# Kernel optimization log

Hardware: AMD Instinct MI355X
Metric: run time of the kernel (lower is better)

The kernel has to match this reference:

```python
import jax, jax.numpy as jnp
import numpy as np

N_PHM = 4  # hypercomplex division


def _kron_weight(phm_rule, W, in_f, out_f):
    # phm_rule: [n, n, n], W: [n, in_f//n, out_f//n]
    # W_full[p*in_n + q, r*out_n + s] = sum_i phm_rule[i,p,r] * W[i,q,s]
    Wf = jnp.einsum('ipr,iqs->pqrs', phm_rule, W)
    return Wf.reshape(in_f, out_f)


def setup_inputs() -> dict:
    key = jax.random.key(0)
    ks = jax.random.split(key, 5)
    T, D, B = 8192, 2048, 512  # tokens, model dim, bottleneck
    n = N_PHM
    x = jax.random.normal(ks[0], (T, D), dtype=jnp.float32)
    phm_rule = jax.random.normal(ks[1], (n, n, n), dtype=jnp.float32) * 0.5
    # glorot-ish scaling for the per-component weights
    W_down = jax.random.normal(ks[2], (n, D // n, B // n), dtype=jnp.float32) * (1.0 / np.sqrt(D))
    b_down = jnp.zeros((B,), dtype=jnp.float32)
    W_up = jax.random.normal(ks[3], (n, B // n, D // n), dtype=jnp.float32) * (1.0 / np.sqrt(B))
    b_up = jnp.zeros((D,), dtype=jnp.float32)
    return {"x": x, "phm_rule": phm_rule, "W_down": W_down, "b_down": b_down,
            "W_up": W_up, "b_up": b_up}


def reference(x, phm_rule, W_down, b_down, W_up, b_up):
    T, D = x.shape
    B = b_down.shape[0]
    Wd = _kron_weight(phm_rule, W_down, D, B)   # [D, B]
    Wu = _kron_weight(phm_rule, W_up, B, D)     # [B, D]
    z = jax.nn.relu(x @ Wd + b_down)            # down-proj + activation
    return z @ Wu + b_up                         # up-proj
```

## Files before the change

### kernel.cpp

```cpp
#include <hip/hip_runtime.h>
#include <hip/hip_bf16.h>
#include <stdint.h>

using bf16 = __hip_bfloat16;
typedef __attribute__((ext_vector_type(8))) short bf16x8;
typedef __attribute__((ext_vector_type(4))) float f32x4;

static __device__ __forceinline__ float b2f(short u) {
  union { float f; unsigned int i; } c;
  c.i = ((unsigned int)(unsigned short)u) << 16;
  return c.f;
}
static __device__ __forceinline__ short f2b(float f) {
  return (short)__bfloat16_as_ushort(__float2bfloat16(f));
}

static __device__ __forceinline__ void cfence() { asm volatile("" ::: "memory"); }
static __device__ __forceinline__ void bar()    { cfence(); __builtin_amdgcn_s_barrier(); cfence(); }

__device__ __forceinline__ void async16(const void* g, void* lds) {
  __builtin_amdgcn_global_load_lds(
      (const __attribute__((address_space(1))) void*)g,
      (__attribute__((address_space(3))) void*)lds, 16, 0, 0);
}

__global__ void build_w(const float* __restrict__ phm,
                        const float* __restrict__ Wd,
                        const float* __restrict__ Wu,
                        bf16* __restrict__ wdT, bf16* __restrict__ wuT) {
  int idx = blockIdx.x * 256 + threadIdx.x;
  if (idx < 1024 * 1024) {
    int n = idx >> 11, k = idx & 2047;
    int r = n >> 7, s = n & 127;
    int p = k >> 9, q = k & 511;
    float v = 0.f;
#pragma unroll
    for (int i = 0; i < 4; ++i)
      v += phm[i * 16 + p * 4 + r] * Wd[i * 65536 + q * 128 + s];
    wdT[idx] = (bf16)v;
  } else {
    int j = idx - 1024 * 1024;
    int d = j >> 9, b = j & 511;
    int r = d >> 9, s = d & 511;
    int p = b >> 7, q = b & 127;
    float v = 0.f;
#pragma unroll
    for (int i = 0; i < 4; ++i)
      v += phm[i * 16 + p * 4 + r] * Wu[i * 65536 + q * 512 + s];
    wuT[j] = (bf16)v;
  }
}

__global__ void zred(const bf16* __restrict__ P, const float* __restrict__ bias,
                     bf16* __restrict__ z) {
  int i = blockIdx.x * 256 + threadIdx.x;
  const int NV = 8192 * 512 / 8;
  if (i >= NV) return;
  const size_t CS = (size_t)NV;
  bf16x8 v0 = ((const bf16x8*)P)[i];
  bf16x8 v1 = ((const bf16x8*)P)[i + CS];
  bf16x8 v2 = ((const bf16x8*)P)[i + 2 * CS];
  bf16x8 v3 = ((const bf16x8*)P)[i + 3 * CS];
  int c0 = (i * 8) & 511;
  bf16x8 o;
#pragma unroll
  for (int j = 0; j < 8; ++j) {
    float t = b2f(v0[j]) + b2f(v1[j]) + b2f(v2[j]) + b2f(v3[j]) + bias[c0 + j];
    o[j] = f2b(t > 0.f ? t : 0.f);
  }
  ((bf16x8*)z)[i] = o;
}

__global__ __launch_bounds__(512, 2)
void gemm1f(const float* __restrict__ X, const bf16* __restrict__ Wt,
            bf16* __restrict__ P) {
  constexpr int BK = 64, KTOT = 2048, NOUT = 512;
  __shared__ bf16 Ash[128 * 64];
  __shared__ bf16 Bsh[2][2][256 * 64];

  const int xcd = blockIdx.x & 7, w = blockIdx.x >> 3;
  const int bx = xcd * 8 + (w & 7);
  const int ch = w >> 3;
  const int bm = bx * 128;
  const int koff = ch * 512;
  bf16* __restrict__ Pc = P + (size_t)ch * 8192 * NOUT;

  const int tid  = threadIdx.x;
  const int lane = tid & 63;
  const int wave = tid >> 6;
  const int wm   = (wave >> 2) * 64;
  const int wnn  = (wave & 3) * 128;
  const int hB   = wnn >> 8;
  const int bb   = wnn & 255;
  const int rl   = lane & 15;
  const int sw   = lane >> 4;
  const int sx   = rl & 7;

  const int arow = tid >> 2;
  const int ac0  = (tid & 3) * 16;
  const float* __restrict__ Xrow = X + (size_t)(bm + arow) * KTOT + koff + ac0;
  const int as0 = (tid & 3) * 2;

  f32x4 acc[4][8] = {};
  float4 av[4];

#define ISSUE_AV(tt)                                                          \
  { _Pragma("unroll")                                                         \
    for (int j = 0; j < 4; ++j)                                               \
      av[j] = *(const float4*)(Xrow + (size_t)(tt) * BK + j * 4); }

#define WRITE_A()                                                             \
  {                                                                           \
    bf16x8 w0, w1;                                                            \
    _Pragma("unroll")                                                         \
    for (int e = 0; e < 4; ++e) {                                             \
      w0[e]     = f2b(((const float*)&av[0])[e]);                             \
      w0[e + 4] = f2b(((const float*)&av[1])[e]);                             \
      w1[e]     = f2b(((const float*)&av[2])[e]);                             \
      w1[e + 4] = f2b(((const float*)&av[3])[e]);                             \
    }                                                                         \
    *(bf16x8*)(&Ash[arow * 64 + (((as0)     ^ (arow & 7)) * 8)]) = w0;        \
    *(bf16x8*)(&Ash[arow * 64 + (((as0 + 1) ^ (arow & 7)) * 8)]) = w1;        \
  }

#define STAGE_BH(tt, h)                                                       \
  { _Pragma("unroll")                                                         \
    for (int is = 0; is < 4; ++is) {                                          \
      int idx = is * 512 + tid;                                               \
      int r = idx >> 3, sl = idx & 7;                                         \
      async16(Wt + (size_t)((h) * 256 + r) * KTOT + koff + (tt) * BK          \
                  + ((sl ^ (r & 7)) * 8),                                     \
              &Bsh[(tt) & 1][h][idx * 8]);                                    \
    } }

  const int nt = 512 / BK;

  ISSUE_AV(0);
  STAGE_BH(0, 0); STAGE_BH(0, 1);
  asm volatile("s_waitcnt vmcnt(8)" ::: "memory");
  WRITE_A();
  ISSUE_AV(1);
  asm volatile("s_waitcnt vmcnt(4) lgkmcnt(0)" ::: "memory");
  bar();

  bf16x8 af[4][2], bfr[2][2];

  for (int t = 0; t < nt; ++t) {
    const int cur = t & 1;
    const bf16* __restrict__ Bcur = &Bsh[cur][hB][0];

#define LDAF(m, ks) af[m][ks] = *(const bf16x8*)(&Ash[(wm + (m)*16 + rl) * 64 + ((((ks)*4 + sw) ^ sx) * 8)])
#define LDBF(j, n, ks) bfr[j][ks] = *(const bf16x8*)(Bcur + (bb + (n)*16 + rl) * 64 + ((((ks)*4 + sw) ^ sx) * 8))
#define QUAD(N0)                                                              \
  __builtin_amdgcn_s_setprio(1);                                              \
  _Pragma("unroll") for (int m = 0; m < 4; ++m)                               \
  _Pragma("unroll") for (int n = 0; n < 2; ++n)                               \
  _Pragma("unroll") for (int ks = 0; ks < 2; ++ks)                            \
    acc[m][(N0) + n] = __builtin_amdgcn_mfma_f32_16x16x32_bf16(               \
        af[m][ks], bfr[n][ks], acc[m][(N0) + n], 0, 0, 0);                    \
  __builtin_amdgcn_s_setprio(0);

    LDAF(0, 0); LDAF(0, 1); LDAF(1, 0); LDAF(1, 1);
    LDAF(2, 0); LDAF(2, 1); LDAF(3, 0); LDAF(3, 1);
    LDBF(0, 0, 0); LDBF(0, 0, 1); LDBF(1, 1, 0); LDBF(1, 1, 1);
    cfence();
    if (t + 1 < nt) STAGE_BH(t + 1, 0);
    bar(); QUAD(0); bar();
    LDBF(0, 2, 0); LDBF(0, 2, 1); LDBF(1, 3, 0); LDBF(1, 3, 1);
    cfence();
    if (t + 1 < nt) STAGE_BH(t + 1, 1);
    bar(); QUAD(2); bar();
    LDBF(0, 4, 0); LDBF(0, 4, 1); LDBF(1, 5, 0); LDBF(1, 5, 1);
    cfence();
    bar(); QUAD(4); bar();
    LDBF(0, 6, 0); LDBF(0, 6, 1); LDBF(1, 7, 0); LDBF(1, 7, 1);
    cfence();
    if (t + 1 < nt) {
      asm volatile("s_waitcnt vmcnt(8)" ::: "memory");
      WRITE_A();
      if (t + 2 < nt) {
        ISSUE_AV(t + 2);
        asm volatile("s_waitcnt vmcnt(4) lgkmcnt(0)" ::: "memory");
      } else {
        asm volatile("s_waitcnt vmcnt(0) lgkmcnt(0)" ::: "memory");
      }
    }
    __builtin_amdgcn_sched_barrier(0);
    bar(); QUAD(6);
    if (t + 1 < nt) bar();

#undef LDAF
#undef LDBF
#undef QUAD
  }
#undef ISSUE_AV
#undef WRITE_A
#undef STAGE_BH

  float* scr = (float*)(&Bsh[0][0][0]) + wave * (16 * 128);
#pragma unroll
  for (int m = 0; m < 4; ++m) {
    int grow = bm + wm + m * 16;
#pragma unroll
    for (int n = 0; n < 8; ++n)
#pragma unroll
      for (int j = 0; j < 4; ++j)
        scr[(sw * 4 + j) * 128 + n * 16 + rl] = acc[m][n][j];
    asm volatile("s_waitcnt lgkmcnt(0)" ::: "memory");
#pragma unroll
    for (int p = 0; p < 4; ++p) {
      int row = p * 4 + sw;
      f32x4 a = *(const f32x4*)(scr + row * 128 + rl * 8);
      f32x4 b = *(const f32x4*)(scr + row * 128 + rl * 8 + 4);
      bf16x8 o;
#pragma unroll
      for (int e = 0; e < 4; ++e) { o[e] = f2b(a[e]); o[e + 4] = f2b(b[e]); }
      *(bf16x8*)(&Pc[(size_t)(grow + row) * NOUT + wnn + rl * 8]) = o;
    }
    asm volatile("s_waitcnt lgkmcnt(0)" ::: "memory");
  }
}

__global__ __launch_bounds__(512, 2)
void gemm2(const bf16* __restrict__ A, const bf16* __restrict__ Bt,
           const float* __restrict__ bias, float* __restrict__ Cout) {
  constexpr int BK = 64, LDA = 512, LDB = 512, N = 2048;
  __shared__ bf16 Ash[2][2][128 * 64];
  __shared__ bf16 Bsh[2][2][128 * 64];

  const int xcd = blockIdx.x & 7, w = blockIdx.x >> 3;
  const int bx = xcd * 4 + (w & 3);
  const int by = w >> 2;
  const int bm = bx * 256;
  const int bn = by * 256;

  const int tid  = threadIdx.x;
  const int lane = tid & 63;
  const int wave = tid >> 6;
  const int wmh  = wave >> 2;
  const int wn   = wave & 3;
  const int wnh  = wn >> 1;
  const int brow = (wn & 1) * 64;
  const int rl   = lane & 15;
  const int sw   = lane >> 4;
  const int sx   = rl & 7;

  f32x4 acc[8][4] = {};

#define STAGE_A(tt, h)                                                        \
  { _Pragma("unroll")                                                         \
    for (int is = 0; is < 2; ++is) {                                          \
      int idx = is * 512 + tid;                                               \
      int r = idx >> 3, sl = idx & 7;                                         \
      async16(A + (size_t)(bm + (h) * 128 + r) * LDA + (tt) * BK              \
                  + ((sl ^ (r & 7)) * 8),                                     \
              &Ash[(tt) & 1][h][idx * 8]);                                    \
    } }
#define STAGE_B(tt, h)                                                        \
  { _Pragma("unroll")                                                         \
    for (int is = 0; is < 2; ++is) {                                          \
      int idx = is * 512 + tid;                                               \
      int r = idx >> 3, sl = idx & 7;                                         \
      async16(Bt + (size_t)(bn + (h) * 128 + r) * LDB + (tt) * BK             \
                  + ((sl ^ (r & 7)) * 8),                                     \
              &Bsh[(tt) & 1][h][idx * 8]);                                    \
    } }

  const int nt = 512 / BK;

  STAGE_A(0, 0); STAGE_A(0, 1);
  STAGE_B(0, 0); STAGE_B(0, 1);
  STAGE_A(1, 0); STAGE_A(1, 1);
  asm volatile("s_waitcnt vmcnt(4)" ::: "memory");
  bar();

  bf16x8 af[8][2], bf[4][2];

  for (int t = 0; t < nt; ++t) {
    const int cur = t & 1;
    const bf16* __restrict__ Acur = &Ash[cur][wmh][0];
    const bf16* __restrict__ Bcur = &Bsh[cur][wnh][0];

#define LDA_(m, ks) af[m][ks] = *(const bf16x8*)(Acur + ((m)*16 + rl) * 64 + ((((ks)*4 + sw) ^ sx) * 8))
#define LDB_(n, ks) bf[n][ks] = *(const bf16x8*)(Bcur + (brow + (n)*16 + rl) * 64 + ((((ks)*4 + sw) ^ sx) * 8))
#define QUAD(M0, N0)                                                          \
  __builtin_amdgcn_s_setprio(1);                                              \
  _Pragma("unroll") for (int m = 0; m < 4; ++m)                               \
  _Pragma("unroll") for (int n = 0; n < 2; ++n)                               \
  _Pragma("unroll") for (int ks = 0; ks < 2; ++ks)                            \
    acc[(M0) + m][(N0) + n] = __builtin_amdgcn_mfma_f32_16x16x32_bf16(        \
        af[(M0) + m][ks], bf[(N0) + n][ks], acc[(M0) + m][(N0) + n], 0, 0, 0);\
  __builtin_amdgcn_s_setprio(0);

    LDA_(0, 0); LDA_(0, 1); LDA_(1, 0); LDA_(1, 1);
    LDA_(2, 0); LDA_(2, 1); LDA_(3, 0); LDA_(3, 1);
    LDB_(0, 0); LDB_(0, 1); LDB_(1, 0); LDB_(1, 1);
    cfence();
    if (t + 1 < nt) STAGE_B(t + 1, 0);
    bar(); QUAD(0, 0); bar();
    LDB_(2, 0); LDB_(2, 1); LDB_(3, 0); LDB_(3, 1);
    cfence();
    if (t + 1 < nt) STAGE_B(t + 1, 1);
    bar(); QUAD(0, 2); bar();
    LDA_(4, 0); LDA_(4, 1); LDA_(5, 0); LDA_(5, 1);
    LDA_(6, 0); LDA_(6, 1); LDA_(7, 0); LDA_(7, 1);
    cfence();
    bar(); QUAD(4, 0); bar();
    if (t + 2 < nt) {
      STAGE_A(t + 2, 0); STAGE_A(t + 2, 1);
      asm volatile("s_waitcnt vmcnt(4)" ::: "memory");
    } else if (t + 1 < nt) {
      asm volatile("s_waitcnt vmcnt(0)" ::: "memory");
    }
    bar(); QUAD(4, 2);
    if (t + 1 < nt) bar();

#undef LDA_
#undef LDB_
#undef QUAD
  }
#undef STAGE_A
#undef STAGE_B

  float* scr = (float*)(&Ash[0][0][0]) + wave * (16 * 68);
  const int r4 = lane >> 4;
  const int c4 = lane & 15;
#pragma unroll
  for (int m = 0; m < 8; ++m) {
    int grow = bm + wmh * 128 + m * 16;
#pragma unroll
    for (int n = 0; n < 4; ++n)
#pragma unroll
      for (int j = 0; j < 4; ++j)
        scr[(sw * 4 + j) * 68 + n * 16 + rl] = acc[m][n][j] + bias[bn + wn * 64 + n * 16 + rl];
    asm volatile("s_waitcnt lgkmcnt(0)" ::: "memory");
#pragma unroll
    for (int jj = 0; jj < 4; ++jj) {
      int row = jj * 4 + r4;
      f32x4 v = *(const f32x4*)(scr + row * 68 + c4 * 4);
      *(f32x4*)(&Cout[(size_t)(grow + row) * N + bn + wn * 64 + c4 * 4]) = v;
    }
    asm volatile("s_waitcnt lgkmcnt(0)" ::: "memory");
  }
}

extern "C" void kernel_launch(void* const* d_in, const int* in_sizes, int n_in,
                              void* d_out, int out_size, void* d_ws, size_t ws_size,
                              hipStream_t stream) {
  const float* x      = (const float*)d_in[0];
  const float* phm    = (const float*)d_in[1];
  const float* W_down = (const float*)d_in[2];
  const float* b_down = (const float*)d_in[3];
  const float* W_up   = (const float*)d_in[4];
  const float* b_up   = (const float*)d_in[5];
  float* out = (float*)d_out;

  const int T = 8192, B = 512;
  const size_t MB = 1024 * 1024;

  char* ws = (char*)d_ws;
  bf16* wdT = (bf16*)(ws);
  bf16* wuT = (bf16*)(ws + 2 * MB);
  bf16* z   = (bf16*)(ws + 4 * MB);
  bf16* P   = (bf16*)(ws + 12 * MB);

  build_w<<<dim3((2 * 1024 * 1024) / 256), dim3(256), 0, stream>>>(
      phm, W_down, W_up, wdT, wuT);

  gemm1f<<<dim3(256), dim3(512), 0, stream>>>(x, wdT, P);

  zred<<<dim3(T * B / 8 / 256), dim3(256), 0, stream>>>(P, b_down, z);

  gemm2<<<dim3(256), dim3(512), 0, stream>>>(z, wuT, b_up, out);
}
```

Measured before the change: 96.93 us.

## Fuse gemm1, reduction and gemm2 into one persistent kernel with flag sync

Merges the split-K down-projection GEMM, the partial-sum reduction with bias and ReLU, and the up-projection GEMM into a single kernel. The last of the four split-K blocks for a row group performs the reduction and publishes a flag, and gemm2 blocks spin on flags for their two row groups before consuming Z. This removes two kernel launches and the gaps between them, and lets gemm2 start on ready rows early. The cost is a memset, spin-waits that depend on all 256 blocks being co-resident, and extra serialization in the reducer blocks. Output stores also become nontemporal.

```diff
diff --git a/kernel.cpp b/kernel.cpp
--- a/kernel.cpp
+++ b/kernel.cpp
@@ -39,75 +39,57 @@
       v += phm[i * 16 + p * 4 + r] * Wd[i * 65536 + q * 128 + s];
     wdT[idx] = (bf16)v;
   } else {
-    int j = idx - 1024 * 1024;
-    int d = j >> 9, b = j & 511;
+    int jj = idx - 1024 * 1024;
+    int d = jj >> 9, b = jj & 511;
     int r = d >> 9, s = d & 511;
     int p = b >> 7, q = b & 127;
     float v = 0.f;
 #pragma unroll
     for (int i = 0; i < 4; ++i)
       v += phm[i * 16 + p * 4 + r] * Wu[i * 65536 + q * 512 + s];
-    wuT[j] = (bf16)v;
-  }
-}
-
-__global__ void zred(const bf16* __restrict__ P, const float* __restrict__ bias,
-                     bf16* __restrict__ z) {
-  int i = blockIdx.x * 256 + threadIdx.x;
-  const int NV = 8192 * 512 / 8;
-  if (i >= NV) return;
-  const size_t CS = (size_t)NV;
-  bf16x8 v0 = ((const bf16x8*)P)[i];
-  bf16x8 v1 = ((const bf16x8*)P)[i + CS];
-  bf16x8 v2 = ((const bf16x8*)P)[i + 2 * CS];
-  bf16x8 v3 = ((const bf16x8*)P)[i + 3 * CS];
-  int c0 = (i * 8) & 511;
-  bf16x8 o;
-#pragma unroll
-  for (int j = 0; j < 8; ++j) {
-    float t = b2f(v0[j]) + b2f(v1[j]) + b2f(v2[j]) + b2f(v3[j]) + bias[c0 + j];
-    o[j] = f2b(t > 0.f ? t : 0.f);
-  }
-  ((bf16x8*)z)[i] = o;
+    wuT[jj] = (bf16)v;
+  }
 }
 
 __global__ __launch_bounds__(512, 2)
-void gemm1f(const float* __restrict__ X, const bf16* __restrict__ Wt,
-            bf16* __restrict__ P) {
-  constexpr int BK = 64, KTOT = 2048, NOUT = 512;
-  __shared__ bf16 Ash[128 * 64];
-  __shared__ bf16 Bsh[2][2][256 * 64];
-
-  const int xcd = blockIdx.x & 7, w = blockIdx.x >> 3;
-  const int bx = xcd * 8 + (w & 7);
-  const int ch = w >> 3;
-  const int bm = bx * 128;
-  const int koff = ch * 512;
-  bf16* __restrict__ Pc = P + (size_t)ch * 8192 * NOUT;
-
-  const int tid  = threadIdx.x;
-  const int lane = tid & 63;
-  const int wave = tid >> 6;
-  const int wm   = (wave >> 2) * 64;
-  const int wnn  = (wave & 3) * 128;
-  const int hB   = wnn >> 8;
-  const int bb   = wnn & 255;
-  const int rl   = lane & 15;
-  const int sw   = lane >> 4;
-  const int sx   = rl & 7;
-
-  const int arow = tid >> 2;
-  const int ac0  = (tid & 3) * 16;
-  const float* __restrict__ Xrow = X + (size_t)(bm + arow) * KTOT + koff + ac0;
-  const int as0 = (tid & 3) * 2;
-
-  f32x4 acc[4][8] = {};
-  float4 av[4];
+void fused(const float* __restrict__ X, const bf16* __restrict__ wdT,
+           const bf16* __restrict__ wuT, const float* __restrict__ bd,
+           const float* __restrict__ bu, bf16* __restrict__ P,
+           bf16* __restrict__ Z, float* __restrict__ OUT,
+           int* __restrict__ cnt, int* __restrict__ flags) {
+  __shared__ bf16 BIG[2][2][256 * 64];
+  __shared__ bf16 A1[128 * 64];
+  __shared__ int amLastSh;
+
+  const int bid = blockIdx.x;
+  const int x8 = bid & 7, j = bid >> 3;
+  const int tid = threadIdx.x, lane = tid & 63, wave = tid >> 6;
+  const int rl = lane & 15, sw = lane >> 4, sx = rl & 7;
+  const int rg1 = x8 * 8 + (j & 7);
+
+  {
+    const int ch = j >> 3;
+    const int bm = rg1 * 128;
+    const int koff = ch * 512;
+    bf16* __restrict__ Pc = P + (size_t)ch * (8192 * 512);
+
+    const int wm  = (wave >> 2) * 64;
+    const int wnn = (wave & 3) * 128;
+    const int hB  = wnn >> 8;
+    const int bb  = wnn & 255;
+
+    const int arow = tid >> 2;
+    const int ac0  = (tid & 3) * 16;
+    const float* __restrict__ Xrow = X + (size_t)(bm + arow) * 2048 + koff + ac0;
+    const int as0 = (tid & 3) * 2;
+
+    f32x4 acc[4][8] = {};
+    float4 av[4];
 
 #define ISSUE_AV(tt)                                                          \
   { _Pragma("unroll")                                                         \
-    for (int j = 0; j < 4; ++j)                                               \
-      av[j] = *(const float4*)(Xrow + (size_t)(tt) * BK + j * 4); }
+    for (int q = 0; q < 4; ++q)                                               \
+      av[q] = *(const float4*)(Xrow + (size_t)(tt) * 64 + q * 4); }
 
 #define WRITE_A()                                                             \
   {                                                                           \
@@ -119,8 +101,8 @@
       w1[e]     = f2b(((const float*)&av[2])[e]);                             \
       w1[e + 4] = f2b(((const float*)&av[3])[e]);                             \
     }                                                                         \
-    *(bf16x8*)(&Ash[arow * 64 + (((as0)     ^ (arow & 7)) * 8)]) = w0;        \
-    *(bf16x8*)(&Ash[arow * 64 + (((as0 + 1) ^ (arow & 7)) * 8)]) = w1;        \
+    *(bf16x8*)(&A1[arow * 64 + (((as0)     ^ (arow & 7)) * 8)]) = w0;         \
+    *(bf16x8*)(&A1[arow * 64 + (((as0 + 1) ^ (arow & 7)) * 8)]) = w1;         \
   }
 
 #define STAGE_BH(tt, h)                                                       \
@@ -128,30 +110,30 @@
     for (int is = 0; is < 4; ++is) {                                          \
       int idx = is * 512 + tid;                                               \
       int r = idx >> 3, sl = idx & 7;                                         \
-      async16(Wt + (size_t)((h) * 256 + r) * KTOT + koff + (tt) * BK          \
+      async16(wdT + (size_t)((h) * 256 + r) * 2048 + koff + (tt) * 64         \
                   + ((sl ^ (r & 7)) * 8),                                     \
-              &Bsh[(tt) & 1][h][idx * 8]);                                    \
+              &BIG[(tt) & 1][h][idx * 8]);                                    \
     } }
 
-  const int nt = 512 / BK;
-
-  ISSUE_AV(0);
-  STAGE_BH(0, 0); STAGE_BH(0, 1);
-  asm volatile("s_waitcnt vmcnt(8)" ::: "memory");
-  WRITE_A();
-  ISSUE_AV(1);
-  asm volatile("s_waitcnt vmcnt(4) lgkmcnt(0)" ::: "memory");
-  bar();
-
-  bf16x8 af[4][2], bfr[2][2];
-
-  for (int t = 0; t < nt; ++t) {
-    const int cur = t & 1;
-    const bf16* __restrict__ Bcur = &Bsh[cur][hB][0];
-
-#define LDAF(m, ks) af[m][ks] = *(const bf16x8*)(&Ash[(wm + (m)*16 + rl) * 64 + ((((ks)*4 + sw) ^ sx) * 8)])
-#define LDBF(j, n, ks) bfr[j][ks] = *(const bf16x8*)(Bcur + (bb + (n)*16 + rl) * 64 + ((((ks)*4 + sw) ^ sx) * 8))
-#define QUAD(N0)                                                              \
+    const int nt = 8;
+
+    ISSUE_AV(0);
+    STAGE_BH(0, 0); STAGE_BH(0, 1);
+    asm volatile("s_waitcnt vmcnt(8)" ::: "memory");
+    WRITE_A();
+    ISSUE_AV(1);
+    asm volatile("s_waitcnt vmcnt(4) lgkmcnt(0)" ::: "memory");
+    bar();
+
+    bf16x8 af[4][2], bfr[2][2];
+
+    for (int t = 0; t < nt; ++t) {
+      const int cur = t & 1;
+      const bf16* __restrict__ Bcur = &BIG[cur][hB][0];
+
+#define LDAF(m, ks) af[m][ks] = *(const bf16x8*)(&A1[(wm + (m)*16 + rl) * 64 + ((((ks)*4 + sw) ^ sx) * 8)])
+#define LDBF(q, n, ks) bfr[q][ks] = *(const bf16x8*)(Bcur + (bb + (n)*16 + rl) * 64 + ((((ks)*4 + sw) ^ sx) * 8))
+#define QUAD1(N0)                                                             \
   __builtin_amdgcn_s_setprio(1);                                              \
   _Pragma("unroll") for (int m = 0; m < 4; ++m)                               \
   _Pragma("unroll") for (int n = 0; n < 2; ++n)                               \
@@ -160,130 +142,164 @@
         af[m][ks], bfr[n][ks], acc[m][(N0) + n], 0, 0, 0);                    \
   __builtin_amdgcn_s_setprio(0);
 
-    LDAF(0, 0); LDAF(0, 1); LDAF(1, 0); LDAF(1, 1);
-    LDAF(2, 0); LDAF(2, 1); LDAF(3, 0); LDAF(3, 1);
-    LDBF(0, 0, 0); LDBF(0, 0, 1); LDBF(1, 1, 0); LDBF(1, 1, 1);
-    cfence();
-    if (t + 1 < nt) STAGE_BH(t + 1, 0);
-    bar(); QUAD(0); bar();
-    LDBF(0, 2, 0); LDBF(0, 2, 1); LDBF(1, 3, 0); LDBF(1, 3, 1);
-    cfence();
-    if (t + 1 < nt) STAGE_BH(t + 1, 1);
-    bar(); QUAD(2); bar();
-    LDBF(0, 4, 0); LDBF(0, 4, 1); LDBF(1, 5, 0); LDBF(1, 5, 1);
-    cfence();
-    bar(); QUAD(4); bar();
-    LDBF(0, 6, 0); LDBF(0, 6, 1); LDBF(1, 7, 0); LDBF(1, 7, 1);
-    cfence();
-    if (t + 1 < nt) {
-      asm volatile("s_waitcnt vmcnt(8)" ::: "memory");
-      WRITE_A();
-      if (t + 2 < nt) {
-        ISSUE_AV(t + 2);
-        asm volatile("s_waitcnt vmcnt(4) lgkmcnt(0)" ::: "memory");
-      } else {
-        asm volatile("s_waitcnt vmcnt(0) lgkmcnt(0)" ::: "memory");
-      }
-    }
-    __builtin_amdgcn_sched_barrier(0);
-    bar(); QUAD(6);
-    if (t + 1 < nt) bar();
+      LDAF(0, 0); LDAF(0, 1); LDAF(1, 0); LDAF(1, 1);
+      LDAF(2, 0); LDAF(2, 1); LDAF(3, 0); LDAF(3, 1);
+      LDBF(0, 0, 0); LDBF(0, 0, 1); LDBF(1, 1, 0); LDBF(1, 1, 1);
+      cfence();
+      if (t + 1 < nt) STAGE_BH(t + 1, 0);
+      bar(); QUAD1(0); bar();
+      LDBF(0, 2, 0); LDBF(0, 2, 1); LDBF(1, 3, 0); LDBF(1, 3, 1);
+      cfence();
+      if (t + 1 < nt) STAGE_BH(t + 1, 1);
+      bar(); QUAD1(2); bar();
+      LDBF(0, 4, 0); LDBF(0, 4, 1); LDBF(1, 5, 0); LDBF(1, 5, 1);
+      cfence();
+      bar(); QUAD1(4); bar();
+      LDBF(0, 6, 0); LDBF(0, 6, 1); LDBF(1, 7, 0); LDBF(1, 7, 1);
+      cfence();
+      if (t + 1 < nt) {
+        asm volatile("s_waitcnt vmcnt(8)" ::: "memory");
+        WRITE_A();
+        if (t + 2 < nt) {
+          ISSUE_AV(t + 2);
+          asm volatile("s_waitcnt vmcnt(4) lgkmcnt(0)" ::: "memory");
+        } else {
+          asm volatile("s_waitcnt vmcnt(0) lgkmcnt(0)" ::: "memory");
+        }
+      }
+      __builtin_amdgcn_sched_barrier(0);
+      bar(); QUAD1(6);
+      if (t + 1 < nt) bar();
 
 #undef LDAF
 #undef LDBF
-#undef QUAD
-  }
+#undef QUAD1
+    }
 #undef ISSUE_AV
 #undef WRITE_A
 #undef STAGE_BH
 
-  float* scr = (float*)(&Bsh[0][0][0]) + wave * (16 * 128);
-#pragma unroll
-  for (int m = 0; m < 4; ++m) {
-    int grow = bm + wm + m * 16;
-#pragma unroll
-    for (int n = 0; n < 8; ++n)
-#pragma unroll
-      for (int j = 0; j < 4; ++j)
-        scr[(sw * 4 + j) * 128 + n * 16 + rl] = acc[m][n][j];
-    asm volatile("s_waitcnt lgkmcnt(0)" ::: "memory");
-#pragma unroll
-    for (int p = 0; p < 4; ++p) {
-      int row = p * 4 + sw;
-      f32x4 a = *(const f32x4*)(scr + row * 128 + rl * 8);
-      f32x4 b = *(const f32x4*)(scr + row * 128 + rl * 8 + 4);
+    float* scr = (float*)(&BIG[0][0][0]) + wave * (16 * 128);
+#pragma unroll
+    for (int m = 0; m < 4; ++m) {
+      int grow = bm + wm + m * 16;
+#pragma unroll
+      for (int n = 0; n < 8; ++n)
+#pragma unroll
+        for (int q = 0; q < 4; ++q)
+          scr[(sw * 4 + q) * 128 + n * 16 + rl] = acc[m][n][q];
+      asm volatile("s_waitcnt lgkmcnt(0)" ::: "memory");
+#pragma unroll
+      for (int p = 0; p < 4; ++p) {
+        int row = p * 4 + sw;
+        f32x4 a = *(const f32x4*)(scr + row * 128 + rl * 8);
+        f32x4 b = *(const f32x4*)(scr + row * 128 + rl * 8 + 4);
+        bf16x8 o;
+#pragma unroll
+        for (int e = 0; e < 4; ++e) { o[e] = f2b(a[e]); o[e + 4] = f2b(b[e]); }
+        *(bf16x8*)(&Pc[(size_t)(grow + row) * 512 + wnn + rl * 8]) = o;
+      }
+      asm volatile("s_waitcnt lgkmcnt(0)" ::: "memory");
+    }
+  }
+
+  asm volatile("s_waitcnt vmcnt(0)" ::: "memory");
+  __threadfence();
+  if (tid == 0) {
+    int old = atomicAdd(&cnt[rg1], 1);
+    amLastSh = (old == 3) ? 1 : 0;
+  }
+  __syncthreads();
+  if (amLastSh) {
+    __threadfence();
+    const bf16x8* P8 = (const bf16x8*)P;
+    bf16x8* Z8 = (bf16x8*)Z;
+    const size_t CS = (size_t)8192 * 512 / 8;
+    const size_t base = (size_t)rg1 * 128 * 64;
+    for (int i = tid; i < 128 * 64; i += 512) {
+      size_t idx = base + i;
+      bf16x8 a = P8[idx], b = P8[idx + CS], c = P8[idx + 2 * CS], d = P8[idx + 3 * CS];
+      int c0 = (i & 63) * 8;
       bf16x8 o;
 #pragma unroll
-      for (int e = 0; e < 4; ++e) { o[e] = f2b(a[e]); o[e + 4] = f2b(b[e]); }
-      *(bf16x8*)(&Pc[(size_t)(grow + row) * NOUT + wnn + rl * 8]) = o;
-    }
-    asm volatile("s_waitcnt lgkmcnt(0)" ::: "memory");
-  }
-}
-
-__global__ __launch_bounds__(512, 2)
-void gemm2(const bf16* __restrict__ A, const bf16* __restrict__ Bt,
-           const float* __restrict__ bias, float* __restrict__ Cout) {
-  constexpr int BK = 64, LDA = 512, LDB = 512, N = 2048;
-  __shared__ bf16 Ash[2][2][128 * 64];
-  __shared__ bf16 Bsh[2][2][128 * 64];
-
-  const int xcd = blockIdx.x & 7, w = blockIdx.x >> 3;
-  const int bx = xcd * 4 + (w & 3);
-  const int by = w >> 2;
-  const int bm = bx * 256;
-  const int bn = by * 256;
-
-  const int tid  = threadIdx.x;
-  const int lane = tid & 63;
-  const int wave = tid >> 6;
-  const int wmh  = wave >> 2;
-  const int wn   = wave & 3;
-  const int wnh  = wn >> 1;
-  const int brow = (wn & 1) * 64;
-  const int rl   = lane & 15;
-  const int sw   = lane >> 4;
-  const int sx   = rl & 7;
-
-  f32x4 acc[8][4] = {};
-
-#define STAGE_A(tt, h)                                                        \
+      for (int e = 0; e < 8; ++e) {
+        float t = b2f(a[e]) + b2f(b[e]) + b2f(c[e]) + b2f(d[e]) + bd[c0 + e];
+        o[e] = f2b(t > 0.f ? t : 0.f);
+      }
+      Z8[idx] = o;
+    }
+    asm volatile("s_waitcnt vmcnt(0)" ::: "memory");
+    __threadfence();
+    if (tid == 0)
+      __hip_atomic_store(&flags[rg1], 1, __ATOMIC_RELAXED, __HIP_MEMORY_SCOPE_AGENT);
+  }
+
+  const int bx2 = x8 * 4 + (j & 3);
+  const int by2 = j >> 2;
+  if (tid == 0) {
+    while (__hip_atomic_load(&flags[bx2 * 2], __ATOMIC_RELAXED,
+                             __HIP_MEMORY_SCOPE_AGENT) == 0)
+      __builtin_amdgcn_s_sleep(1);
+    while (__hip_atomic_load(&flags[bx2 * 2 + 1], __ATOMIC_RELAXED,
+                             __HIP_MEMORY_SCOPE_AGENT) == 0)
+      __builtin_amdgcn_s_sleep(1);
+  }
+  __syncthreads();
+  __threadfence();
+  bar();
+
+  {
+    const int bm = bx2 * 256;
+    const int bn = by2 * 256;
+    const int wmh  = wave >> 2;
+    const int wn2  = wave & 3;
+    const int wnh  = wn2 >> 1;
+    const int brow = (wn2 & 1) * 64;
+
+    bf16* const A2 = &BIG[0][0][0];
+    bf16* const B2 = &BIG[1][0][0];
+#define ASH2(buf, half) (A2 + ((buf) * 2 + (half)) * 8192)
+#define BSH2(buf, half) (B2 + ((buf) * 2 + (half)) * 8192)
+
+    f32x4 acc[8][4] = {};
+
+#define STAGE_A2(tt, h)                                                       \
   { _Pragma("unroll")                                                         \
     for (int is = 0; is < 2; ++is) {                                          \
       int idx = is * 512 + tid;                                               \
       int r = idx >> 3, sl = idx & 7;                                         \
-      async16(A + (size_t)(bm + (h) * 128 + r) * LDA + (tt) * BK              \
+      async16(Z + (size_t)(bm + (h) * 128 + r) * 512 + (tt) * 64              \
                   + ((sl ^ (r & 7)) * 8),                                     \
-              &Ash[(tt) & 1][h][idx * 8]);                                    \
+              ASH2((tt) & 1, h) + idx * 8);                                   \
     } }
-#define STAGE_B(tt, h)                                                        \
+#define STAGE_B2(tt, h)                                                       \
   { _Pragma("unroll")                                                         \
     for (int is = 0; is < 2; ++is) {                                          \
       int idx = is * 512 + tid;                                               \
       int r = idx >> 3, sl = idx & 7;                                         \
-      async16(Bt + (size_t)(bn + (h) * 128 + r) * LDB + (tt) * BK             \
+      async16(wuT + (size_t)(bn + (h) * 128 + r) * 512 + (tt) * 64            \
                   + ((sl ^ (r & 7)) * 8),                                     \
-              &Bsh[(tt) & 1][h][idx * 8]);                                    \
+              BSH2((tt) & 1, h) + idx * 8);                                   \
     } }
 
-  const int nt = 512 / BK;
-
-  STAGE_A(0, 0); STAGE_A(0, 1);
-  STAGE_B(0, 0); STAGE_B(0, 1);
-  STAGE_A(1, 0); STAGE_A(1, 1);
-  asm volatile("s_waitcnt vmcnt(4)" ::: "memory");
-  bar();
-
-  bf16x8 af[8][2], bf[4][2];
-
-  for (int t = 0; t < nt; ++t) {
-    const int cur = t & 1;
-    const bf16* __restrict__ Acur = &Ash[cur][wmh][0];
-    const bf16* __restrict__ Bcur = &Bsh[cur][wnh][0];
-
-#define LDA_(m, ks) af[m][ks] = *(const bf16x8*)(Acur + ((m)*16 + rl) * 64 + ((((ks)*4 + sw) ^ sx) * 8))
-#define LDB_(n, ks) bf[n][ks] = *(const bf16x8*)(Bcur + (brow + (n)*16 + rl) * 64 + ((((ks)*4 + sw) ^ sx) * 8))
-#define QUAD(M0, N0)                                                          \
+    const int nt = 8;
+
+    STAGE_A2(0, 0); STAGE_A2(0, 1);
+    STAGE_B2(0, 0); STAGE_B2(0, 1);
+    STAGE_A2(1, 0); STAGE_A2(1, 1);
+    asm volatile("s_waitcnt vmcnt(4)" ::: "memory");
+    bar();
+
+    bf16x8 af[8][2], bf[4][2];
+
+    for (int t = 0; t < nt; ++t) {
+      const int cur = t & 1;
+      const bf16* __restrict__ Acur = ASH2(cur, wmh);
+      const bf16* __restrict__ Bcur = BSH2(cur, wnh);
+
+#define LDA2(m, ks) af[m][ks] = *(const bf16x8*)(Acur + ((m)*16 + rl) * 64 + ((((ks)*4 + sw) ^ sx) * 8))
+#define LDB2(n, ks) bf[n][ks] = *(const bf16x8*)(Bcur + (brow + (n)*16 + rl) * 64 + ((((ks)*4 + sw) ^ sx) * 8))
+#define QUAD2(M0, N0)                                                         \
   __builtin_amdgcn_s_setprio(1);                                              \
   _Pragma("unroll") for (int m = 0; m < 4; ++m)                               \
   _Pragma("unroll") for (int n = 0; n < 2; ++n)                               \
@@ -292,55 +308,60 @@
         af[(M0) + m][ks], bf[(N0) + n][ks], acc[(M0) + m][(N0) + n], 0, 0, 0);\
   __builtin_amdgcn_s_setprio(0);
 
-    LDA_(0, 0); LDA_(0, 1); LDA_(1, 0); LDA_(1, 1);
-    LDA_(2, 0); LDA_(2, 1); LDA_(3, 0); LDA_(3, 1);
-    LDB_(0, 0); LDB_(0, 1); LDB_(1, 0); LDB_(1, 1);
-    cfence();
-    if (t + 1 < nt) STAGE_B(t + 1, 0);
-    bar(); QUAD(0, 0); bar();
-    LDB_(2, 0); LDB_(2, 1); LDB_(3, 0); LDB_(3, 1);
-    cfence();
-    if (t + 1 < nt) STAGE_B(t + 1, 1);
-    bar(); QUAD(0, 2); bar();
-    LDA_(4, 0); LDA_(4, 1); LDA_(5, 0); LDA_(5, 1);
-    LDA_(6, 0); LDA_(6, 1); LDA_(7, 0); LDA_(7, 1);
-    cfence();
-    bar(); QUAD(4, 0); bar();
-    if (t + 2 < nt) {
-      STAGE_A(t + 2, 0); STAGE_A(t + 2, 1);
-      asm volatile("s_waitcnt vmcnt(4)" ::: "memory");
-    } else if (t + 1 < nt) {
-      asm volatile("s_waitcnt vmcnt(0)" ::: "memory");
-    }
-    bar(); QUAD(4, 2);
-    if (t + 1 < nt) bar();
-
-#undef LDA_
-#undef LDB_
-#undef QUAD
-  }
-#undef STAGE_A
-#undef STAGE_B
-
-  float* scr = (float*)(&Ash[0][0][0]) + wave * (16 * 68);
-  const int r4 = lane >> 4;
-  const int c4 = lane & 15;
-#pragma unroll
-  for (int m = 0; m < 8; ++m) {
-    int grow = bm + wmh * 128 + m * 16;
-#pragma unroll
-    for (int n = 0; n < 4; ++n)
-#pragma unroll
-      for (int j = 0; j < 4; ++j)
-        scr[(sw * 4 + j) * 68 + n * 16 + rl] = acc[m][n][j] + bias[bn + wn * 64 + n * 16 + rl];
-    asm volatile("s_waitcnt lgkmcnt(0)" ::: "memory");
-#pragma unroll
-    for (int jj = 0; jj < 4; ++jj) {
-      int row = jj * 4 + r4;
-      f32x4 v = *(const f32x4*)(scr + row * 68 + c4 * 4);
-      *(f32x4*)(&Cout[(size_t)(grow + row) * N + bn + wn * 64 + c4 * 4]) = v;
-    }
-    asm volatile("s_waitcnt lgkmcnt(0)" ::: "memory");
+      LDA2(0, 0); LDA2(0, 1); LDA2(1, 0); LDA2(1, 1);
+      LDA2(2, 0); LDA2(2, 1); LDA2(3, 0); LDA2(3, 1);
+      LDB2(0, 0); LDB2(0, 1); LDB2(1, 0); LDB2(1, 1);
+      cfence();
+      if (t + 1 < nt) STAGE_B2(t + 1, 0);
+      bar(); QUAD2(0, 0); bar();
+      LDB2(2, 0); LDB2(2, 1); LDB2(3, 0); LDB2(3, 1);
+      cfence();
+      if (t + 1 < nt) STAGE_B2(t + 1, 1);
+      bar(); QUAD2(0, 2); bar();
+      LDA2(4, 0); LDA2(4, 1); LDA2(5, 0); LDA2(5, 1);
+      LDA2(6, 0); LDA2(6, 1); LDA2(7, 0); LDA2(7, 1);
+      cfence();
+      bar(); QUAD2(4, 0); bar();
+      if (t + 2 < nt) {
+        STAGE_A2(t + 2, 0); STAGE_A2(t + 2, 1);
+        asm volatile("s_waitcnt vmcnt(4)" ::: "memory");
+      } else if (t + 1 < nt) {
+        asm volatile("s_waitcnt vmcnt(0)" ::: "memory");
+      }
+      bar(); QUAD2(4, 2);
+      if (t + 1 < nt) bar();
+
+#undef LDA2
+#undef LDB2
+#undef QUAD2
+    }
+#undef STAGE_A2
+#undef STAGE_B2
+
+    float* scr = (float*)A2 + wave * (16 * 68);
+    const int r4 = lane >> 4;
+    const int c4 = lane & 15;
+#pragma unroll
+    for (int m = 0; m < 8; ++m) {
+      int grow = bm + wmh * 128 + m * 16;
+#pragma unroll
+      for (int n = 0; n < 4; ++n)
+#pragma unroll
+        for (int q = 0; q < 4; ++q)
+          scr[(sw * 4 + q) * 68 + n * 16 + rl] =
+              acc[m][n][q] + bu[bn + wn2 * 64 + n * 16 + rl];
+      asm volatile("s_waitcnt lgkmcnt(0)" ::: "memory");
+#pragma unroll
+      for (int jj = 0; jj < 4; ++jj) {
+        int row = jj * 4 + r4;
+        f32x4 v = *(const f32x4*)(scr + row * 68 + c4 * 4);
+        __builtin_nontemporal_store(
+            v, (f32x4*)(&OUT[(size_t)(grow + row) * 2048 + bn + wn2 * 64 + c4 * 4]));
+      }
+      asm volatile("s_waitcnt lgkmcnt(0)" ::: "memory");
+    }
+#undef ASH2
+#undef BSH2
   }
 }
 
@@ -355,21 +376,19 @@
   const float* b_up   = (const float*)d_in[5];
   float* out = (float*)d_out;
 
-  const int T = 8192, B = 512;
   const size_t MB = 1024 * 1024;
-
   char* ws = (char*)d_ws;
   bf16* wdT = (bf16*)(ws);
   bf16* wuT = (bf16*)(ws + 2 * MB);
   bf16* z   = (bf16*)(ws + 4 * MB);
   bf16* P   = (bf16*)(ws + 12 * MB);
+  int*  sync = (int*)(ws + 44 * MB);
+
+  hipMemsetAsync(sync, 0, 128 * sizeof(int), stream);
 
   build_w<<<dim3((2 * 1024 * 1024) / 256), dim3(256), 0, stream>>>(
       phm, W_down, W_up, wdT, wuT);
 
-  gemm1f<<<dim3(256), dim3(512), 0, stream>>>(x, wdT, P);
-
-  zred<<<dim3(T * B / 8 / 256), dim3(256), 0, stream>>>(P, b_down, z);
-
-  gemm2<<<dim3(256), dim3(512), 0, stream>>>(z, wuT, b_up, out);
-}
+  fused<<<dim3(256), dim3(512), 0, stream>>>(
+      x, wdT, wuT, b_down, b_up, P, z, out, sync, sync + 64);
+}
```

After: 199.4 us. 106% more time.

## Fuse split-K partial reduction and ReLU into second GEMM's A-tile load

Applied to the files above, without the earlier changes.

Removes the separate zred kernel. The second GEMM now loads the four split-K bf16 partials of the first GEMM directly, sums them, applies ReLU and writes the result to LDS as its A operand. To keep the bias correct, each partial chunk adds a quarter of the down bias in the first GEMM's epilogue. The output store becomes nontemporal. This cuts a kernel launch and the write and read of the z buffer, but gemm2 now reads four times more A data per tile and issues it synchronously through registers instead of async LDS loads.

```diff
diff --git a/kernel.cpp b/kernel.cpp
--- a/kernel.cpp
+++ b/kernel.cpp
@@ -39,41 +39,21 @@
       v += phm[i * 16 + p * 4 + r] * Wd[i * 65536 + q * 128 + s];
     wdT[idx] = (bf16)v;
   } else {
-    int j = idx - 1024 * 1024;
-    int d = j >> 9, b = j & 511;
+    int jj = idx - 1024 * 1024;
+    int d = jj >> 9, b = jj & 511;
     int r = d >> 9, s = d & 511;
     int p = b >> 7, q = b & 127;
     float v = 0.f;
 #pragma unroll
     for (int i = 0; i < 4; ++i)
       v += phm[i * 16 + p * 4 + r] * Wu[i * 65536 + q * 512 + s];
-    wuT[j] = (bf16)v;
-  }
-}
-
-__global__ void zred(const bf16* __restrict__ P, const float* __restrict__ bias,
-                     bf16* __restrict__ z) {
-  int i = blockIdx.x * 256 + threadIdx.x;
-  const int NV = 8192 * 512 / 8;
-  if (i >= NV) return;
-  const size_t CS = (size_t)NV;
-  bf16x8 v0 = ((const bf16x8*)P)[i];
-  bf16x8 v1 = ((const bf16x8*)P)[i + CS];
-  bf16x8 v2 = ((const bf16x8*)P)[i + 2 * CS];
-  bf16x8 v3 = ((const bf16x8*)P)[i + 3 * CS];
-  int c0 = (i * 8) & 511;
-  bf16x8 o;
-#pragma unroll
-  for (int j = 0; j < 8; ++j) {
-    float t = b2f(v0[j]) + b2f(v1[j]) + b2f(v2[j]) + b2f(v3[j]) + bias[c0 + j];
-    o[j] = f2b(t > 0.f ? t : 0.f);
-  }
-  ((bf16x8*)z)[i] = o;
+    wuT[jj] = (bf16)v;
+  }
 }
 
 __global__ __launch_bounds__(512, 2)
 void gemm1f(const float* __restrict__ X, const bf16* __restrict__ Wt,
-            bf16* __restrict__ P) {
+            const float* __restrict__ bd, bf16* __restrict__ P) {
   constexpr int BK = 64, KTOT = 2048, NOUT = 512;
   __shared__ bf16 Ash[128 * 64];
   __shared__ bf16 Bsh[2][2][256 * 64];
@@ -83,7 +63,7 @@
   const int ch = w >> 3;
   const int bm = bx * 128;
   const int koff = ch * 512;
-  bf16* __restrict__ Pc = P + (size_t)ch * 8192 * NOUT;
+  bf16* __restrict__ Pc = P + (size_t)ch * (8192 * NOUT);
 
   const int tid  = threadIdx.x;
   const int lane = tid & 63;
@@ -106,8 +86,8 @@
 
 #define ISSUE_AV(tt)                                                          \
   { _Pragma("unroll")                                                         \
-    for (int j = 0; j < 4; ++j)                                               \
-      av[j] = *(const float4*)(Xrow + (size_t)(tt) * BK + j * 4); }
+    for (int q = 0; q < 4; ++q)                                               \
+      av[q] = *(const float4*)(Xrow + (size_t)(tt) * BK + q * 4); }
 
 #define WRITE_A()                                                             \
   {                                                                           \
@@ -119,7 +99,7 @@
       w1[e]     = f2b(((const float*)&av[2])[e]);                             \
       w1[e + 4] = f2b(((const float*)&av[3])[e]);                             \
     }                                                                         \
-    *(bf16x8*)(&Ash[arow * 64 + (((as0)     ^ (arow & 7)) * 8)]) = w0;        \
+    *(bf16x8*)(&Ash[arow * 64 + ((as0 ^ (arow & 7)) * 8)]) = w0;              \
     *(bf16x8*)(&Ash[arow * 64 + (((as0 + 1) ^ (arow & 7)) * 8)]) = w1;        \
   }
 
@@ -150,8 +130,8 @@
     const bf16* __restrict__ Bcur = &Bsh[cur][hB][0];
 
 #define LDAF(m, ks) af[m][ks] = *(const bf16x8*)(&Ash[(wm + (m)*16 + rl) * 64 + ((((ks)*4 + sw) ^ sx) * 8)])
-#define LDBF(j, n, ks) bfr[j][ks] = *(const bf16x8*)(Bcur + (bb + (n)*16 + rl) * 64 + ((((ks)*4 + sw) ^ sx) * 8))
-#define QUAD(N0)                                                              \
+#define LDBF(q, n, ks) bfr[q][ks] = *(const bf16x8*)(Bcur + (bb + (n)*16 + rl) * 64 + ((((ks)*4 + sw) ^ sx) * 8))
+#define QUAD1(N0)                                                             \
   __builtin_amdgcn_s_setprio(1);                                              \
   _Pragma("unroll") for (int m = 0; m < 4; ++m)                               \
   _Pragma("unroll") for (int n = 0; n < 2; ++n)                               \
@@ -165,14 +145,14 @@
     LDBF(0, 0, 0); LDBF(0, 0, 1); LDBF(1, 1, 0); LDBF(1, 1, 1);
     cfence();
     if (t + 1 < nt) STAGE_BH(t + 1, 0);
-    bar(); QUAD(0); bar();
+    bar(); QUAD1(0); bar();
     LDBF(0, 2, 0); LDBF(0, 2, 1); LDBF(1, 3, 0); LDBF(1, 3, 1);
     cfence();
     if (t + 1 < nt) STAGE_BH(t + 1, 1);
-    bar(); QUAD(2); bar();
+    bar(); QUAD1(2); bar();
     LDBF(0, 4, 0); LDBF(0, 4, 1); LDBF(1, 5, 0); LDBF(1, 5, 1);
     cfence();
-    bar(); QUAD(4); bar();
+    bar(); QUAD1(4); bar();
     LDBF(0, 6, 0); LDBF(0, 6, 1); LDBF(1, 7, 0); LDBF(1, 7, 1);
     cfence();
     if (t + 1 < nt) {
@@ -186,17 +166,21 @@
       }
     }
     __builtin_amdgcn_sched_barrier(0);
-    bar(); QUAD(6);
+    bar(); QUAD1(6);
     if (t + 1 < nt) bar();
 
 #undef LDAF
 #undef LDBF
-#undef QUAD
+#undef QUAD1
   }
 #undef ISSUE_AV
 #undef WRITE_A
 #undef STAGE_BH
 
+  float bv[8];
+#pragma unroll
+  for (int n = 0; n < 8; ++n) bv[n] = 0.25f * bd[wnn + n * 16 + rl];
+
   float* scr = (float*)(&Bsh[0][0][0]) + wave * (16 * 128);
 #pragma unroll
   for (int m = 0; m < 4; ++m) {
@@ -204,8 +188,8 @@
 #pragma unroll
     for (int n = 0; n < 8; ++n)
 #pragma unroll
-      for (int j = 0; j < 4; ++j)
-        scr[(sw * 4 + j) * 128 + n * 16 + rl] = acc[m][n][j];
+      for (int q = 0; q < 4; ++q)
+        scr[(sw * 4 + q) * 128 + n * 16 + rl] = acc[m][n][q] + bv[n];
     asm volatile("s_waitcnt lgkmcnt(0)" ::: "memory");
 #pragma unroll
     for (int p = 0; p < 4; ++p) {
@@ -222,9 +206,9 @@
 }
 
 __global__ __launch_bounds__(512, 2)
-void gemm2(const bf16* __restrict__ A, const bf16* __restrict__ Bt,
-           const float* __restrict__ bias, float* __restrict__ Cout) {
-  constexpr int BK = 64, LDA = 512, LDB = 512, N = 2048;
+void gemm2f(const bf16* __restrict__ P, const bf16* __restrict__ Bt,
+            const float* __restrict__ bu, float* __restrict__ OUT) {
+  constexpr int LDB = 512, N = 2048;
   __shared__ bf16 Ash[2][2][128 * 64];
   __shared__ bf16 Bsh[2][2][128 * 64];
 
@@ -234,47 +218,58 @@
   const int bm = bx * 256;
   const int bn = by * 256;
 
-  const int tid  = threadIdx.x;
-  const int lane = tid & 63;
-  const int wave = tid >> 6;
-  const int wmh  = wave >> 2;
-  const int wn   = wave & 3;
-  const int wnh  = wn >> 1;
-  const int brow = (wn & 1) * 64;
-  const int rl   = lane & 15;
-  const int sw   = lane >> 4;
-  const int sx   = rl & 7;
+  const int tid = threadIdx.x, lane = tid & 63, wave = tid >> 6;
+  const int wmh = wave >> 2;
+  const int wn2 = wave & 3;
+  const int wnh = wn2 >> 1;
+  const int brow = (wn2 & 1) * 64;
+  const int rl = lane & 15, sw = lane >> 4, sx = rl & 7;
+
+  const int arow = tid >> 1, ac0 = (tid & 1) * 32;
+  const int ah = arow >> 7, ar = arow & 127;
+  const int as0 = (tid & 1) * 4;
+  const size_t CS = (size_t)8192 * 512;
+  const bf16* __restrict__ Pr = P + (size_t)(bm + arow) * 512 + ac0;
 
   f32x4 acc[8][4] = {};
-
-#define STAGE_A(tt, h)                                                        \
-  { _Pragma("unroll")                                                         \
-    for (int is = 0; is < 2; ++is) {                                          \
-      int idx = is * 512 + tid;                                               \
-      int r = idx >> 3, sl = idx & 7;                                         \
-      async16(A + (size_t)(bm + (h) * 128 + r) * LDA + (tt) * BK              \
-                  + ((sl ^ (r & 7)) * 8),                                     \
-              &Ash[(tt) & 1][h][idx * 8]);                                    \
+  bf16x8 avv[4][4];
+  bf16x8 af[8][2], bf[4][2];
+
+#define ISSUE_A(tt)                                                           \
+  { _Pragma("unroll") for (int c = 0; c < 4; ++c)                             \
+    _Pragma("unroll") for (int s = 0; s < 4; ++s)                             \
+      avv[c][s] = *(const bf16x8*)(Pr + c * CS + (tt) * 64 + s * 8); }
+
+#define WRITE_A(buf)                                                          \
+  { _Pragma("unroll") for (int s = 0; s < 4; ++s) {                           \
+      bf16x8 o;                                                               \
+      _Pragma("unroll") for (int e = 0; e < 8; ++e) {                         \
+        float v = b2f(avv[0][s][e]) + b2f(avv[1][s][e]) +                     \
+                  b2f(avv[2][s][e]) + b2f(avv[3][s][e]);                      \
+        o[e] = f2b(v > 0.f ? v : 0.f);                                        \
+      }                                                                       \
+      *(bf16x8*)(&Ash[buf][ah][ar * 64 + (((as0 + s) ^ (ar & 7)) * 8)]) = o;  \
     } }
+
 #define STAGE_B(tt, h)                                                        \
   { _Pragma("unroll")                                                         \
     for (int is = 0; is < 2; ++is) {                                          \
       int idx = is * 512 + tid;                                               \
       int r = idx >> 3, sl = idx & 7;                                         \
-      async16(Bt + (size_t)(bn + (h) * 128 + r) * LDB + (tt) * BK             \
+      async16(Bt + (size_t)(bn + (h) * 128 + r) * LDB + (tt) * 64             \
                   + ((sl ^ (r & 7)) * 8),                                     \
               &Bsh[(tt) & 1][h][idx * 8]);                                    \
     } }
 
-  const int nt = 512 / BK;
-
-  STAGE_A(0, 0); STAGE_A(0, 1);
+  const int nt = 8;
+
+  ISSUE_A(0);
+  asm volatile("s_waitcnt vmcnt(0)" ::: "memory");
+  WRITE_A(0);
   STAGE_B(0, 0); STAGE_B(0, 1);
-  STAGE_A(1, 0); STAGE_A(1, 1);
-  asm volatile("s_waitcnt vmcnt(4)" ::: "memory");
+  ISSUE_A(1);
+  asm volatile("s_waitcnt vmcnt(16) lgkmcnt(0)" ::: "memory");
   bar();
-
-  bf16x8 af[8][2], bf[4][2];
 
   for (int t = 0; t < nt; ++t) {
     const int cur = t & 1;
@@ -283,7 +278,7 @@
 
 #define LDA_(m, ks) af[m][ks] = *(const bf16x8*)(Acur + ((m)*16 + rl) * 64 + ((((ks)*4 + sw) ^ sx) * 8))
 #define LDB_(n, ks) bf[n][ks] = *(const bf16x8*)(Bcur + (brow + (n)*16 + rl) * 64 + ((((ks)*4 + sw) ^ sx) * 8))
-#define QUAD(M0, N0)                                                          \
+#define QUAD2(M0, N0)                                                         \
   __builtin_amdgcn_s_setprio(1);                                              \
   _Pragma("unroll") for (int m = 0; m < 4; ++m)                               \
   _Pragma("unroll") for (int n = 0; n < 2; ++n)                               \
@@ -297,29 +292,36 @@
     LDB_(0, 0); LDB_(0, 1); LDB_(1, 0); LDB_(1, 1);
     cfence();
     if (t + 1 < nt) STAGE_B(t + 1, 0);
-    bar(); QUAD(0, 0); bar();
+    bar(); QUAD2(0, 0); bar();
     LDB_(2, 0); LDB_(2, 1); LDB_(3, 0); LDB_(3, 1);
     cfence();
     if (t + 1 < nt) STAGE_B(t + 1, 1);
-    bar(); QUAD(0, 2); bar();
+    bar(); QUAD2(0, 2); bar();
     LDA_(4, 0); LDA_(4, 1); LDA_(5, 0); LDA_(5, 1);
     LDA_(6, 0); LDA_(6, 1); LDA_(7, 0); LDA_(7, 1);
     cfence();
-    bar(); QUAD(4, 0); bar();
-    if (t + 2 < nt) {
-      STAGE_A(t + 2, 0); STAGE_A(t + 2, 1);
+    bar(); QUAD2(4, 0); bar();
+    if (t + 1 < nt) {
       asm volatile("s_waitcnt vmcnt(4)" ::: "memory");
-    } else if (t + 1 < nt) {
-      asm volatile("s_waitcnt vmcnt(0)" ::: "memory");
+      WRITE_A((t + 1) & 1);
+      if (t + 2 < nt) {
+        ISSUE_A(t + 2);
+        asm volatile("s_waitcnt vmcnt(16) lgkmcnt(0)" ::: "memory");
+      } else {
+        asm volatile("s_waitcnt vmcnt(0) lgkmcnt(0)" ::: "memory");
+      }
+      __builtin_amdgcn_sched_barrier(0);
+      bar();
     }
-    bar(); QUAD(4, 2);
+    QUAD2(4, 2);
     if (t + 1 < nt) bar();
 
 #undef LDA_
 #undef LDB_
-#undef QUAD
-  }
-#undef STAGE_A
+#undef QUAD2
+  }
+#undef ISSUE_A
+#undef WRITE_A
 #undef STAGE_B
 
   float* scr = (float*)(&Ash[0][0][0]) + wave * (16 * 68);
@@ -331,14 +333,16 @@
 #pragma unroll
     for (int n = 0; n < 4; ++n)
 #pragma unroll
-      for (int j = 0; j < 4; ++j)
-        scr[(sw * 4 + j) * 68 + n * 16 + rl] = acc[m][n][j] + bias[bn + wn * 64 + n * 16 + rl];
+      for (int q = 0; q < 4; ++q)
+        scr[(sw * 4 + q) * 68 + n * 16 + rl] =
+            acc[m][n][q] + bu[bn + wn2 * 64 + n * 16 + rl];
     asm volatile("s_waitcnt lgkmcnt(0)" ::: "memory");
 #pragma unroll
     for (int jj = 0; jj < 4; ++jj) {
       int row = jj * 4 + r4;
       f32x4 v = *(const f32x4*)(scr + row * 68 + c4 * 4);
-      *(f32x4*)(&Cout[(size_t)(grow + row) * N + bn + wn * 64 + c4 * 4]) = v;
+      __builtin_nontemporal_store(
+          v, (f32x4*)(&OUT[(size_t)(grow + row) * N + bn + wn2 * 64 + c4 * 4]));
     }
     asm volatile("s_waitcnt lgkmcnt(0)" ::: "memory");
   }
@@ -355,21 +359,16 @@
   const float* b_up   = (const float*)d_in[5];
   float* out = (float*)d_out;
 
-  const int T = 8192, B = 512;
   const size_t MB = 1024 * 1024;
-
   char* ws = (char*)d_ws;
   bf16* wdT = (bf16*)(ws);
   bf16* wuT = (bf16*)(ws + 2 * MB);
-  bf16* z   = (bf16*)(ws + 4 * MB);
-  bf16* P   = (bf16*)(ws + 12 * MB);
+  bf16* P   = (bf16*)(ws + 4 * MB);
 
   build_w<<<dim3((2 * 1024 * 1024) / 256), dim3(256), 0, stream>>>(
       phm, W_down, W_up, wdT, wuT);
 
-  gemm1f<<<dim3(256), dim3(512), 0, stream>>>(x, wdT, P);
-
-  zred<<<dim3(T * B / 8 / 256), dim3(256), 0, stream>>>(P, b_down, z);
-
-  gemm2<<<dim3(256), dim3(512), 0, stream>>>(z, wuT, b_up, out);
-}
+  gemm1f<<<dim3(256), dim3(512), 0, stream>>>(x, wdT, b_down, P);
+
+  gemm2f<<<dim3(256), dim3(512), 0, stream>>>(P, wuT, b_up, out);
+}
```

Result: slower. 132.4 us (+36.5%).
